# Optimization experiments

Hardware: AMD Instinct MI355X
Metric: run time of the kernel (lower is better)

The kernel has to match this reference:

```python
import jax, jax.numpy as jnp
import numpy as np

KPS = 256
HID = 1024


def _lstm_cell(x, h, c, w_ih, w_hh, b_ih, b_hh):
    # PyTorch LSTMCell: gates = x@W_ih.T + b_ih + h@W_hh.T + b_hh; order i,f,g,o
    gates = x @ w_ih.T + b_ih + h @ w_hh.T + b_hh  # [B, 4H]
    i, f, g, o = jnp.split(gates, 4, axis=-1)
    i = jax.nn.sigmoid(i)
    f = jax.nn.sigmoid(f)
    g = jnp.tanh(g)
    o = jax.nn.sigmoid(o)
    c_new = f * c + i * g
    h_new = o * jnp.tanh(c_new)
    return h_new, c_new


def setup_inputs() -> dict:
    key = jax.random.key(0)
    ks = jax.random.split(key, 20)
    B = 4096
    s_emb = 1.0 / np.sqrt(KPS)
    s_h = 1.0 / np.sqrt(HID)
    inp = {
        "kps": jax.random.normal(ks[0], (B, KPS), jnp.float32),
        "h0": jax.random.normal(ks[1], (B, HID), jnp.float32),
        "h1": jax.random.normal(ks[2], (B, HID), jnp.float32),
        "h2": jax.random.normal(ks[3], (B, HID), jnp.float32),
        "c0": jax.random.normal(ks[4], (B, HID), jnp.float32),
        "c1": jax.random.normal(ks[5], (B, HID), jnp.float32),
        "c2": jax.random.normal(ks[6], (B, HID), jnp.float32),
        # tgt_emb: Linear(kps_size, kps_size)
        "W_emb": jax.random.uniform(ks[7], (KPS, KPS), jnp.float32, -s_emb, s_emb),
        "b_emb": jax.random.uniform(ks[8], (KPS,), jnp.float32, -s_emb, s_emb),
        # lstm1: input KPS -> HID
        "w_ih1": jax.random.uniform(ks[9], (4 * HID, KPS), jnp.float32, -s_h, s_h),
        "w_hh1": jax.random.uniform(ks[10], (4 * HID, HID), jnp.float32, -s_h, s_h),
        "b_ih1": jax.random.uniform(ks[11], (4 * HID,), jnp.float32, -s_h, s_h),
        "b_hh1": jax.random.uniform(ks[12], (4 * HID,), jnp.float32, -s_h, s_h),
        # lstm2, lstm3: HID -> HID
        "w_ih2": jax.random.uniform(ks[13], (4 * HID, HID), jnp.float32, -s_h, s_h),
        "w_hh2": jax.random.uniform(ks[14], (4 * HID, HID), jnp.float32, -s_h, s_h),
        "b_ih2": jax.random.uniform(ks[15], (4 * HID,), jnp.float32, -s_h, s_h),
        "b_hh2": jax.random.uniform(ks[16], (4 * HID,), jnp.float32, -s_h, s_h),
        "w_ih3": jax.random.uniform(ks[17], (4 * HID, HID), jnp.float32, -s_h, s_h),
        "w_hh3": jax.random.uniform(ks[18], (4 * HID, HID), jnp.float32, -s_h, s_h),
        "b_ih3": jax.random.uniform(ks[19], (4 * HID,), jnp.float32, -s_h, s_h),
        "b_hh3": jax.random.uniform(jax.random.fold_in(key, 99), (4 * HID,), jnp.float32, -s_h, s_h),
    }
    return inp


def reference(kps, h0, h1, h2, c0, c1, c2,
              W_emb, b_emb,
              w_ih1, w_hh1, b_ih1, b_hh1,
              w_ih2, w_hh2, b_ih2, b_hh2,
              w_ih3, w_hh3, b_ih3, b_hh3):
    # tgt_emb linear; dropout is identity in eval mode
    in_frame = kps @ W_emb.T + b_emb
    # NOTE: per original code, lstm2/lstm3 consume the *old* hidden states
    # h0 / h1 (not the freshly computed ones).
    h0n, c0n = _lstm_cell(in_frame, h0, c0, w_ih1, w_hh1, b_ih1, b_hh1)
    h1n, c1n = _lstm_cell(h0, h1, c1, w_ih2, w_hh2, b_ih2, b_hh2)
    h2n, c2n = _lstm_cell(h1, h2, c2, w_ih3, w_hh3, b_ih3, b_hh3)
    return (h2n, h0n, h1n, h2n, c0n, c1n, c2n)
```

## Files before the change

kernel.cpp:

```cpp
#include <hip/hip_runtime.h>
#include <stdint.h>

typedef __bf16 bf16;
typedef __bf16 bf16x8 __attribute__((ext_vector_type(8)));
typedef float f32x4 __attribute__((ext_vector_type(4)));

#define B_DIM 4096
#define HID   1024
#define KPSZ  256

#define BM  128
#define BNH 32
#define BK  64

__device__ __forceinline__ bool detect_b16(const void* kps) {
  const uint16_t* k16 = (const uint16_t*)kps;
  int lane = threadIdx.x & 63;
  int c = 0;
#pragma unroll
  for (int j = 0; j < 8; ++j) {
    uint16_t v = k16[(lane * 8 + j) * 2];
    int e = (v >> 7) & 0xFF;
    c += (e >= 100 && e <= 140) ? 1 : 0;
  }
#pragma unroll
  for (int s = 1; s < 64; s <<= 1) c += __shfl_xor(c, s, 64);
  return c > 256;
}

__device__ __forceinline__ bf16x8 load8(const void* base, size_t off, bool b16) {
  if (b16) {
    return *(const bf16x8*)((const bf16*)base + off);
  } else {
    const float* f = (const float*)base + off;
    float4 lo = *(const float4*)f;
    float4 hi = *(const float4*)(f + 4);
    bf16x8 r;
    r[0] = (bf16)lo.x; r[1] = (bf16)lo.y; r[2] = (bf16)lo.z; r[3] = (bf16)lo.w;
    r[4] = (bf16)hi.x; r[5] = (bf16)hi.y; r[6] = (bf16)hi.z; r[7] = (bf16)hi.w;
    return r;
  }
}
__device__ __forceinline__ float ldg1(const void* p, size_t i, bool b16) {
  return b16 ? (float)((const bf16*)p)[i] : ((const float*)p)[i];
}
__device__ __forceinline__ void stg1(void* p, size_t i, float v, bool b16) {
  if (b16) ((bf16*)p)[i] = (bf16)v;
  else     ((float*)p)[i] = v;
}

__device__ __forceinline__ float sigm(float x) {
  return 1.0f / (1.0f + __expf(-x));
}
__device__ __forceinline__ float tanhx(float x) {
  float e = __expf(-2.0f * fabsf(x));
  float t = (1.0f - e) / (1.0f + e);
  return x < 0.0f ? -t : t;
}

__device__ __forceinline__ int sw(int row, int col8) {
  return row * BK + (col8 ^ ((row & 7) << 3));
}

__device__ __forceinline__ void gl16(const bf16* g, bf16* l) {
  __builtin_amdgcn_global_load_lds(
      (const __attribute__((address_space(1))) void*)g,
      (__attribute__((address_space(3))) void*)l, 16, 0, 0);
}


__global__ __launch_bounds__(256)
void emb_kernel(const void* __restrict__ kps, const void* __restrict__ W,
                const void* __restrict__ bias, void* __restrict__ out) {
  __shared__ __align__(16) bf16 sA[BM * BK];
  __shared__ __align__(16) bf16 sB[BNH * BK];

  const bool b16 = detect_b16(kps);
  const int n0   = blockIdx.x * BNH;
  const int m0   = blockIdx.y * BM;
  const int tid  = threadIdx.x;
  const int wave = tid >> 6;
  const int lane = tid & 63;
  const int l16  = lane & 15;
  const int kg   = lane >> 4;

  f32x4 acc[2][2] = {};

  bf16x8 ra[4], rb;
  #pragma unroll
  for (int i = 0; i < 4; ++i) {
    int it = tid + i * 256;
    ra[i] = load8(kps, (size_t)(m0 + (it >> 3)) * KPSZ + (it & 7) * 8, b16);
  }
  rb = load8(W, (size_t)(n0 + (tid >> 3)) * KPSZ + (tid & 7) * 8, b16);

  for (int s = 0; s < KPSZ / BK; ++s) {
    __syncthreads();
    #pragma unroll
    for (int i = 0; i < 4; ++i) {
      int it = tid + i * 256;
      *(bf16x8*)(sA + sw(it >> 3, (it & 7) * 8)) = ra[i];
    }
    *(bf16x8*)(sB + sw(tid >> 3, (tid & 7) * 8)) = rb;
    __syncthreads();

    if (s + 1 < KPSZ / BK) {
      int k0 = (s + 1) * BK;
      #pragma unroll
      for (int i = 0; i < 4; ++i) {
        int it = tid + i * 256;
        ra[i] = load8(kps, (size_t)(m0 + (it >> 3)) * KPSZ + k0 + (it & 7) * 8, b16);
      }
      rb = load8(W, (size_t)(n0 + (tid >> 3)) * KPSZ + k0 + (tid & 7) * 8, b16);
    }

    #pragma unroll
    for (int ks = 0; ks < 2; ++ks) {
      bf16x8 a[2], b[2];
      #pragma unroll
      for (int mi = 0; mi < 2; ++mi) {
        int row = wave * 32 + mi * 16 + l16;
        a[mi] = *(const bf16x8*)(sA + sw(row, ks * 32 + kg * 8));
      }
      #pragma unroll
      for (int ni = 0; ni < 2; ++ni) {
        int row = ni * 16 + l16;
        b[ni] = *(const bf16x8*)(sB + sw(row, ks * 32 + kg * 8));
      }
      #pragma unroll
      for (int mi = 0; mi < 2; ++mi)
        #pragma unroll
        for (int ni = 0; ni < 2; ++ni)
          acc[mi][ni] = __builtin_amdgcn_mfma_f32_16x16x32_bf16(a[mi], b[ni], acc[mi][ni], 0, 0, 0);
    }
  }

  #pragma unroll
  for (int mi = 0; mi < 2; ++mi)
    #pragma unroll
    for (int r = 0; r < 4; ++r) {
      int m = m0 + wave * 32 + mi * 16 + kg * 4 + r;
      #pragma unroll
      for (int ni = 0; ni < 2; ++ni) {
        int n = n0 + ni * 16 + l16;
        stg1(out, (size_t)m * KPSZ + n, acc[mi][ni][r] + ldg1(bias, n, b16), b16);
      }
    }
}

struct CellArgs {
  const void *Ax, *Wih, *Ah, *Whh, *bih, *bhh, *Cprev;
  size_t hoff, h2off, coff;
  int Kx, dup;
};
struct Args3 {
  CellArgs c[3];
  void* outbase;
  const void* kps;
};

__global__ __launch_bounds__(256)
void lstm_cells_kernel(Args3 A) {
  __shared__ __align__(16) bf16 sA[BM * BK];
  __shared__ __align__(16) bf16 sW[4 * BNH * BK];

  const CellArgs p = A.c[blockIdx.z];
  const bool b16 = detect_b16(A.kps);
  const int n0   = blockIdx.x * BNH;
  const int m0   = blockIdx.y * BM;
  const int tid  = threadIdx.x;
  const int wave = tid >> 6;
  const int lane = tid & 63;
  const int l16  = lane & 15;
  const int kg   = lane >> 4;

  f32x4 acc[4][2][2] = {};

  const int steps1 = p.Kx / BK;
  const int steps  = steps1 + HID / BK;

  bf16x8 ra[4], rw[4];
  #pragma unroll
  for (int i = 0; i < 4; ++i) {
    int it = tid + i * 256;
    ra[i] = load8(p.Ax, (size_t)(m0 + (it >> 3)) * p.Kx + (it & 7) * 8, b16);
  }
  #pragma unroll
  for (int i = 0; i < 4; ++i) {
    int it = tid + i * 256;
    int rr = it >> 3;
    int grow = (rr >> 5) * HID + n0 + (rr & 31);
    rw[i] = load8(p.Wih, (size_t)grow * p.Kx + (it & 7) * 8, b16);
  }

  for (int s = 0; s < steps; ++s) {
    __syncthreads();
    #pragma unroll
    for (int i = 0; i < 4; ++i) {
      int it = tid + i * 256;
      *(bf16x8*)(sA + sw(it >> 3, (it & 7) * 8)) = ra[i];
    }
    #pragma unroll
    for (int i = 0; i < 4; ++i) {
      int it = tid + i * 256;
      *(bf16x8*)(sW + sw(it >> 3, (it & 7) * 8)) = rw[i];
    }
    __syncthreads();

    if (s + 1 < steps) {
      const void *A_, *W_; int K_, k0_;
      int s2 = s + 1;
      if (s2 < steps1) { A_ = p.Ax; W_ = p.Wih; K_ = p.Kx; k0_ = s2 * BK; }
      else             { A_ = p.Ah; W_ = p.Whh; K_ = HID;  k0_ = (s2 - steps1) * BK; }
      #pragma unroll
      for (int i = 0; i < 4; ++i) {
        int it = tid + i * 256;
        ra[i] = load8(A_, (size_t)(m0 + (it >> 3)) * K_ + k0_ + (it & 7) * 8, b16);
      }
      #pragma unroll
      for (int i = 0; i < 4; ++i) {
        int it = tid + i * 256;
        int rr = it >> 3;
        int grow = (rr >> 5) * HID + n0 + (rr & 31);
        rw[i] = load8(W_, (size_t)grow * K_ + k0_ + (it & 7) * 8, b16);
      }
    }

    #pragma unroll
    for (int ks = 0; ks < 2; ++ks) {
      bf16x8 a[2], b[4][2];
      #pragma unroll
      for (int mi = 0; mi < 2; ++mi) {
        int row = wave * 32 + mi * 16 + l16;
        a[mi] = *(const bf16x8*)(sA + sw(row, ks * 32 + kg * 8));
      }
      #pragma unroll
      for (int g = 0; g < 4; ++g)
        #pragma unroll
        for (int ni = 0; ni < 2; ++ni) {
          int row = g * 32 + ni * 16 + l16;
          b[g][ni] = *(const bf16x8*)(sW + sw(row, ks * 32 + kg * 8));
        }
      #pragma unroll
      for (int g = 0; g < 4; ++g)
        #pragma unroll
        for (int mi = 0; mi < 2; ++mi)
          #pragma unroll
          for (int ni = 0; ni < 2; ++ni)
            acc[g][mi][ni] = __builtin_amdgcn_mfma_f32_16x16x32_bf16(
                a[mi], b[g][ni], acc[g][mi][ni], 0, 0, 0);
    }
  }

  float bsum[4][2];
  #pragma unroll
  for (int g = 0; g < 4; ++g)
    #pragma unroll
    for (int ni = 0; ni < 2; ++ni) {
      int n = n0 + ni * 16 + l16;
      bsum[g][ni] = ldg1(p.bih, g * HID + n, b16) + ldg1(p.bhh, g * HID + n, b16);
    }

  #pragma unroll
  for (int mi = 0; mi < 2; ++mi)
    #pragma unroll
    for (int r = 0; r < 4; ++r) {
      int m = m0 + wave * 32 + mi * 16 + kg * 4 + r;
      size_t rowoff = (size_t)m * HID;
      #pragma unroll
      for (int ni = 0; ni < 2; ++ni) {
        int n = n0 + ni * 16 + l16;
        float xi = acc[0][mi][ni][r] + bsum[0][ni];
        float xf = acc[1][mi][ni][r] + bsum[1][ni];
        float xg = acc[2][mi][ni][r] + bsum[2][ni];
        float xo = acc[3][mi][ni][r] + bsum[3][ni];
        float I = sigm(xi);
        float F = sigm(xf);
        float G = tanhx(xg);
        float O = sigm(xo);
        float c  = ldg1(p.Cprev, rowoff + n, b16);
        float cn = F * c + I * G;
        float hn = O * tanhx(cn);
        stg1(A.outbase, p.coff + rowoff + n, cn, b16);
        stg1(A.outbase, p.hoff + rowoff + n, hn, b16);
        if (p.dup) stg1(A.outbase, p.h2off + rowoff + n, hn, b16);
      }
    }
}


#define NSEG 9

struct PrepArgs {
  const void* src[NSEG];
  bf16*       dst[NSEG];
  unsigned    pre[NSEG + 1];
  const void* kps;
  const void* W_emb;
  const void* b_emb;
  bf16*       in_frame;
  int         nconv;
};

__global__ __launch_bounds__(256)
void prep_kernel(PrepArgs P) {
  const bool b16 = detect_b16(P.kps);
  const int tid = threadIdx.x;
  const int bid = blockIdx.x;

  if (bid < 256) {
    __shared__ __align__(16) bf16 sA[BM * BK];
    __shared__ __align__(16) bf16 sB[BNH * BK];
    const int n0   = (bid & 7) * BNH;
    const int m0   = (bid >> 3) * BM;
    const int wave = tid >> 6;
    const int lane = tid & 63;
    const int l16  = lane & 15;
    const int kg   = lane >> 4;

    f32x4 acc[2][2] = {};
    bf16x8 ra[4], rb;
    #pragma unroll
    for (int i = 0; i < 4; ++i) {
      int it = tid + i * 256;
      ra[i] = load8(P.kps, (size_t)(m0 + (it >> 3)) * KPSZ + (it & 7) * 8, b16);
    }
    rb = load8(P.W_emb, (size_t)(n0 + (tid >> 3)) * KPSZ + (tid & 7) * 8, b16);

    for (int s = 0; s < KPSZ / BK; ++s) {
      __syncthreads();
      #pragma unroll
      for (int i = 0; i < 4; ++i) {
        int it = tid + i * 256;
        *(bf16x8*)(sA + sw(it >> 3, (it & 7) * 8)) = ra[i];
      }
      *(bf16x8*)(sB + sw(tid >> 3, (tid & 7) * 8)) = rb;
      __syncthreads();

      if (s + 1 < KPSZ / BK) {
        int k0 = (s + 1) * BK;
        #pragma unroll
        for (int i = 0; i < 4; ++i) {
          int it = tid + i * 256;
          ra[i] = load8(P.kps, (size_t)(m0 + (it >> 3)) * KPSZ + k0 + (it & 7) * 8, b16);
        }
        rb = load8(P.W_emb, (size_t)(n0 + (tid >> 3)) * KPSZ + k0 + (tid & 7) * 8, b16);
      }

      #pragma unroll
      for (int ks = 0; ks < 2; ++ks) {
        bf16x8 a[2], bfr[2];
        #pragma unroll
        for (int mi = 0; mi < 2; ++mi) {
          int row = wave * 32 + mi * 16 + l16;
          a[mi] = *(const bf16x8*)(sA + sw(row, ks * 32 + kg * 8));
        }
        #pragma unroll
        for (int ni = 0; ni < 2; ++ni) {
          int row = ni * 16 + l16;
          bfr[ni] = *(const bf16x8*)(sB + sw(row, ks * 32 + kg * 8));
        }
        #pragma unroll
        for (int mi = 0; mi < 2; ++mi)
          #pragma unroll
          for (int ni = 0; ni < 2; ++ni)
            acc[mi][ni] = __builtin_amdgcn_mfma_f32_16x16x32_bf16(a[mi], bfr[ni], acc[mi][ni], 0, 0, 0);
      }
    }

    #pragma unroll
    for (int mi = 0; mi < 2; ++mi)
      #pragma unroll
      for (int r = 0; r < 4; ++r) {
        int m = m0 + wave * 32 + mi * 16 + kg * 4 + r;
        #pragma unroll
        for (int ni = 0; ni < 2; ++ni) {
          int n = n0 + ni * 16 + l16;
          P.in_frame[(size_t)m * KPSZ + n] = (bf16)(acc[mi][ni][r] + ldg1(P.b_emb, n, b16));
        }
      }
    return;
  }

  const int cb = bid - 256;
  const unsigned tot = P.pre[NSEG];
  const unsigned stride = (unsigned)P.nconv * 256u;
  for (unsigned c = (unsigned)cb * 256u + (unsigned)tid; c < tot; c += stride) {
    int s = 0;
    #pragma unroll
    for (int k = 0; k < NSEG - 1; ++k) s += (c >= P.pre[k + 1]) ? 1 : 0;
    unsigned lc = c - P.pre[s];
    bf16x8 v = load8(P.src[s], (size_t)lc * 8, b16);
    *(bf16x8*)(P.dst[s] + (size_t)lc * 8) = v;
  }
}

struct NCell {
  const bf16 *Ax, *Wih, *Ah, *Whh;
  const void *bih, *bhh, *Cprev;
  size_t hoff, h2off, coff;
  int Kx, dup;
};
struct NArgs {
  NCell c[3];
  void* outbase;
  const void* kps;
};

__global__ __launch_bounds__(256)
void lstm_fast_kernel(NArgs A) {
  __shared__ __align__(16) bf16 sA[BM * BK];
  __shared__ __align__(16) bf16 sW[4 * BNH * BK];

  const NCell p = A.c[blockIdx.z];
  const bool b16 = detect_b16(A.kps);
  const int n0   = blockIdx.x * BNH;
  const int m0   = blockIdx.y * BM;
  const int tid  = threadIdx.x;
  const int w    = tid >> 6;
  const int lane = tid & 63;
  const int l16  = lane & 15;
  const int kg   = lane >> 4;
  const int wm   = w >> 1;
  const int wn   = w & 1;

  f32x4 acc[4][4] = {};

  const int steps1 = p.Kx / BK;
  const int steps  = steps1 + HID / BK;

  for (int s = 0; s < steps; ++s) {
    const bf16 *A_, *W_; int K_, k0_;
    if (s < steps1) { A_ = p.Ax; W_ = p.Wih; K_ = p.Kx; k0_ = s * BK; }
    else            { A_ = p.Ah; W_ = p.Whh; K_ = HID;  k0_ = (s - steps1) * BK; }

    #pragma unroll
    for (int j = 0; j < 4; ++j) {
      int c0 = (j * 4 + w) * 64;
      int c  = c0 + lane;
      gl16(A_ + (size_t)(m0 + (c >> 3)) * K_ + k0_ + (c & 7) * 8, sA + c0 * 8);
    }
    #pragma unroll
    for (int j = 0; j < 4; ++j) {
      int c0 = (j * 4 + w) * 64;
      int c  = c0 + lane;
      int r  = c >> 3;
      int grow = (r >> 5) * HID + n0 + (r & 31);
      gl16(W_ + (size_t)grow * K_ + k0_ + (c & 7) * 8, sW + c0 * 8);
    }
    __syncthreads();

    #pragma unroll
    for (int ks = 0; ks < 2; ++ks) {
      bf16x8 a[4], b[4];
      #pragma unroll
      for (int mi = 0; mi < 4; ++mi) {
        int row = wm * 64 + mi * 16 + l16;
        a[mi] = *(const bf16x8*)(sA + row * BK + ks * 32 + kg * 8);
      }
      #pragma unroll
      for (int g = 0; g < 4; ++g) {
        int row = g * 32 + wn * 16 + l16;
        b[g] = *(const bf16x8*)(sW + row * BK + ks * 32 + kg * 8);
      }
      #pragma unroll
      for (int g = 0; g < 4; ++g)
        #pragma unroll
        for (int mi = 0; mi < 4; ++mi)
          acc[g][mi] = __builtin_amdgcn_mfma_f32_16x16x32_bf16(a[mi], b[g], acc[g][mi], 0, 0, 0);
    }
    __syncthreads();
  }

  const int n = n0 + wn * 16 + l16;
  float bsum[4];
  #pragma unroll
  for (int g = 0; g < 4; ++g)
    bsum[g] = ldg1(p.bih, g * HID + n, b16) + ldg1(p.bhh, g * HID + n, b16);

  #pragma unroll
  for (int mi = 0; mi < 4; ++mi)
    #pragma unroll
    for (int r = 0; r < 4; ++r) {
      int m = m0 + wm * 64 + mi * 16 + kg * 4 + r;
      size_t rowoff = (size_t)m * HID;
      float xi = acc[0][mi][r] + bsum[0];
      float xf = acc[1][mi][r] + bsum[1];
      float xg = acc[2][mi][r] + bsum[2];
      float xo = acc[3][mi][r] + bsum[3];
      float I = sigm(xi);
      float F = sigm(xf);
      float G = tanhx(xg);
      float O = sigm(xo);
      float c  = ldg1(p.Cprev, rowoff + n, b16);
      float cn = F * c + I * G;
      float hn = O * tanhx(cn);
      stg1(A.outbase, p.coff + rowoff + n, cn, b16);
      stg1(A.outbase, p.hoff + rowoff + n, hn, b16);
      if (p.dup) stg1(A.outbase, p.h2off + rowoff + n, hn, b16);
    }
}

extern "C" void kernel_launch(void* const* d_in, const int* in_sizes, int n_in,
                              void* d_out, int out_size, void* d_ws, size_t ws_size,
                              hipStream_t stream) {
  const void* kps   = d_in[0];
  const void* h0    = d_in[1];
  const void* h1    = d_in[2];
  const void* h2    = d_in[3];
  const void* c0    = d_in[4];
  const void* c1    = d_in[5];
  const void* c2    = d_in[6];
  const void* W_emb = d_in[7];
  const void* b_emb = d_in[8];
  const void* w_ih1 = d_in[9];
  const void* w_hh1 = d_in[10];
  const void* b_ih1 = d_in[11];
  const void* b_hh1 = d_in[12];
  const void* w_ih2 = d_in[13];
  const void* w_hh2 = d_in[14];
  const void* b_ih2 = d_in[15];
  const void* b_hh2 = d_in[16];
  const void* w_ih3 = d_in[17];
  const void* w_hh3 = d_in[18];
  const void* b_ih3 = d_in[19];
  const void* b_hh3 = d_in[20];

  const size_t S = (size_t)B_DIM * HID;

  const size_t E_SMALL = (size_t)4 * HID * KPSZ;
  const size_t E_BIG   = (size_t)4 * HID * HID;
  const size_t TOT_ELEMS = 2 * E_SMALL + 8 * E_BIG;
  const size_t NEED = TOT_ELEMS * 2;

  if (ws_size >= NEED) {
    bf16* wsb      = (bf16*)d_ws;
    bf16* in_frame = wsb;
    bf16* W1x      = wsb + E_SMALL;
    bf16* W1h      = W1x + E_SMALL;
    bf16* W2x      = W1h + E_BIG;
    bf16* W2h      = W2x + E_BIG;
    bf16* W3x      = W2h + E_BIG;
    bf16* W3h      = W3x + E_BIG;
    bf16* H0       = W3h + E_BIG;
    bf16* H1       = H0 + E_BIG;
    bf16* H2       = H1 + E_BIG;

    PrepArgs P;
    const void* srcs[NSEG] = { w_ih1, w_hh1, w_ih2, w_hh2, w_ih3, w_hh3, h0, h1, h2 };
    bf16*       dsts[NSEG] = { W1x,   W1h,   W2x,   W2h,   W3x,   W3h,  H0, H1, H2 };
    unsigned    cnts[NSEG] = { (unsigned)(E_SMALL / 8), (unsigned)(E_BIG / 8),
                               (unsigned)(E_BIG / 8),   (unsigned)(E_BIG / 8),
                               (unsigned)(E_BIG / 8),   (unsigned)(E_BIG / 8),
                               (unsigned)(E_BIG / 8),   (unsigned)(E_BIG / 8),
                               (unsigned)(E_BIG / 8) };
    unsigned acc = 0;
    for (int i = 0; i < NSEG; ++i) {
      P.src[i] = srcs[i];
      P.dst[i] = dsts[i];
      P.pre[i] = acc;
      acc += cnts[i];
    }
    P.pre[NSEG] = acc;
    P.kps = kps; P.W_emb = W_emb; P.b_emb = b_emb; P.in_frame = in_frame;
    P.nconv = 2048;

    prep_kernel<<<dim3(256 + 2048), 256, 0, stream>>>(P);

    NArgs N;
    N.outbase = d_out;
    N.kps = kps;
    N.c[0] = { in_frame, W1x, H0, W1h, b_ih1, b_hh1, c0, 1 * S, 0, 4 * S, KPSZ, 0 };
    N.c[1] = { H0,       W2x, H1, W2h, b_ih2, b_hh2, c1, 2 * S, 0, 5 * S, HID,  0 };
    N.c[2] = { H1,       W3x, H2, W3h, b_ih3, b_hh3, c2, 0,     3 * S, 6 * S, HID, 1 };

    lstm_fast_kernel<<<dim3(HID / BNH, B_DIM / BM, 3), 256, 0, stream>>>(N);
    return;
  }

  void* in_frame = d_ws;
  emb_kernel<<<dim3(KPSZ / BNH, B_DIM / BM), 256, 0, stream>>>(kps, W_emb, b_emb, in_frame);

  Args3 A;
  A.outbase = d_out;
  A.kps = kps;
  A.c[0] = { in_frame, w_ih1, h0, w_hh1, b_ih1, b_hh1, c0,
             1 * S, 0, 4 * S, KPSZ, 0 };
  A.c[1] = { h0, w_ih2, h1, w_hh2, b_ih2, b_hh2, c1,
             2 * S, 0, 5 * S, HID, 0 };
  A.c[2] = { h1, w_ih3, h2, w_hh3, b_ih3, b_hh3, c2,
             0 * S, 3 * S, 6 * S, HID, 1 };

  lstm_cells_kernel<<<dim3(HID / BNH, B_DIM / BM, 3), 256, 0, stream>>>(A);
}
```

Before: 533.8 us.

## Enlarge LSTM GEMM tiles with double-buffered LDS, XOR swizzle and 8 waves

Reworks the fused LSTM gate GEMM to use 256x64-per-gate tiles with 512 threads, a BK of 32, and double-buffered shared memory so the next tile's global loads overlap the current MFMA work. LDS rows use an XOR swizzle to cut bank conflicts, and s_setprio raises wave priority around the MFMA bursts. The goal is more operand reuse per loaded byte and less exposed load latency. In exchange the grid has far fewer blocks, each holding 128 accumulator registers per lane, which can lower occupancy and leave CUs idle.

After: 565.5 us. 1.06x slower.

```diff
diff --git a/kernel.cpp b/kernel.cpp
--- a/kernel.cpp
+++ b/kernel.cpp
@@ -12,6 +12,10 @@
 #define BM  128
 #define BNH 32
 #define BK  64
+
+#define BM2 256
+#define BN2 64
+#define BK2 32
 
 __device__ __forceinline__ bool detect_b16(const void* kps) {
   const uint16_t* k16 = (const uint16_t*)kps;
@@ -395,6 +399,7 @@
   }
 }
 
+
 struct NCell {
   const bf16 *Ax, *Wih, *Ah, *Whh;
   const void *bih, *bhh, *Cprev;
@@ -407,68 +412,106 @@
   const void* kps;
 };
 
-__global__ __launch_bounds__(256)
-void lstm_fast_kernel(NArgs A) {
-  __shared__ __align__(16) bf16 sA[BM * BK];
-  __shared__ __align__(16) bf16 sW[4 * BNH * BK];
-
-  const NCell p = A.c[blockIdx.z];
-  const bool b16 = detect_b16(A.kps);
-  const int n0   = blockIdx.x * BNH;
-  const int m0   = blockIdx.y * BM;
+__device__ __forceinline__ void stage_tile2(const bf16* A_, const bf16* W_,
+                                            int K_, int k0_, int m0, int n0,
+                                            bf16* sa, bf16* swk,
+                                            int w, int lane) {
+  #pragma unroll
+  for (int j = 0; j < 2; ++j) {
+    int c0 = (j * 8 + w) * 64;
+    int c  = c0 + lane;
+    int row = c >> 2, col8 = c & 3;
+    int gc  = col8 ^ ((row >> 1) & 3);
+    gl16(A_ + (size_t)(m0 + row) * K_ + k0_ + gc * 8, sa + c0 * 8);
+  }
+  #pragma unroll
+  for (int j = 0; j < 2; ++j) {
+    int c0 = (j * 8 + w) * 64;
+    int c  = c0 + lane;
+    int row = c >> 2, col8 = c & 3;
+    int gc  = col8 ^ ((row >> 1) & 3);
+    int wrow = (row >> 6) * HID + n0 + (row & 63);
+    gl16(W_ + (size_t)wrow * K_ + k0_ + gc * 8, swk + c0 * 8);
+  }
+}
+
+__global__ __launch_bounds__(512, 2)
+void lstm_fast_kernel(NArgs Ar) {
+  __shared__ __align__(16) bf16 sA[2][BM2 * BK2];
+  __shared__ __align__(16) bf16 sW[2][4 * BN2 * BK2];
+
+  const NCell p = Ar.c[blockIdx.z];
+  const bool b16 = detect_b16(Ar.kps);
+  const int n0   = blockIdx.x * BN2;
+  const int m0   = blockIdx.y * BM2;
   const int tid  = threadIdx.x;
   const int w    = tid >> 6;
   const int lane = tid & 63;
   const int l16  = lane & 15;
   const int kg   = lane >> 4;
-  const int wm   = w >> 1;
-  const int wn   = w & 1;
-
-  f32x4 acc[4][4] = {};
-
-  const int steps1 = p.Kx / BK;
-  const int steps  = steps1 + HID / BK;
-
-  for (int s = 0; s < steps; ++s) {
-    const bf16 *A_, *W_; int K_, k0_;
-    if (s < steps1) { A_ = p.Ax; W_ = p.Wih; K_ = p.Kx; k0_ = s * BK; }
-    else            { A_ = p.Ah; W_ = p.Whh; K_ = HID;  k0_ = (s - steps1) * BK; }
-
-    #pragma unroll
-    for (int j = 0; j < 4; ++j) {
-      int c0 = (j * 4 + w) * 64;
-      int c  = c0 + lane;
-      gl16(A_ + (size_t)(m0 + (c >> 3)) * K_ + k0_ + (c & 7) * 8, sA + c0 * 8);
-    }
-    #pragma unroll
-    for (int j = 0; j < 4; ++j) {
-      int c0 = (j * 4 + w) * 64;
-      int c  = c0 + lane;
-      int r  = c >> 3;
-      int grow = (r >> 5) * HID + n0 + (r & 31);
-      gl16(W_ + (size_t)grow * K_ + k0_ + (c & 7) * 8, sW + c0 * 8);
-    }
-    __syncthreads();
-
-    #pragma unroll
-    for (int ks = 0; ks < 2; ++ks) {
-      bf16x8 a[4], b[4];
+  const int wm   = w >> 2;
+  const int wn   = w & 3;
+
+  f32x4 acc[4][8] = {};
+
+  const int s1 = p.Kx / BK2;
+  const int nt = s1 + HID / BK2;
+
+  stage_tile2(p.Ax, p.Wih, p.Kx, 0, m0, n0, sA[0], sW[0], w, lane);
+  __syncthreads();
+
+  for (int v = 0; v < nt; ++v) {
+    if (v + 1 < nt) {
+      const bf16 *A_, *W_; int K_, k0_;
+      int v2 = v + 1;
+      if (v2 < s1) { A_ = p.Ax; W_ = p.Wih; K_ = p.Kx; k0_ = v2 * BK2; }
+      else         { A_ = p.Ah; W_ = p.Whh; K_ = HID;  k0_ = (v2 - s1) * BK2; }
+      stage_tile2(A_, W_, K_, k0_, m0, n0, sA[v2 & 1], sW[v2 & 1], w, lane);
+    }
+
+    const bf16* sa = sA[v & 1];
+    const bf16* sw_ = sW[v & 1];
+
+    bf16x8 b[4];
+    #pragma unroll
+    for (int g = 0; g < 4; ++g) {
+      int rb = g * 64 + wn * 16 + l16;
+      b[g] = *(const bf16x8*)(sw_ + rb * BK2 + ((kg ^ ((rb >> 1) & 3)) * 8));
+    }
+
+    {
+      bf16x8 a[4];
       #pragma unroll
       for (int mi = 0; mi < 4; ++mi) {
-        int row = wm * 64 + mi * 16 + l16;
-        a[mi] = *(const bf16x8*)(sA + row * BK + ks * 32 + kg * 8);
-      }
-      #pragma unroll
-      for (int g = 0; g < 4; ++g) {
-        int row = g * 32 + wn * 16 + l16;
-        b[g] = *(const bf16x8*)(sW + row * BK + ks * 32 + kg * 8);
-      }
+        int ra = wm * 128 + mi * 16 + l16;
+        a[mi] = *(const bf16x8*)(sa + ra * BK2 + ((kg ^ ((ra >> 1) & 3)) * 8));
+      }
+      __builtin_amdgcn_s_setprio(1);
       #pragma unroll
       for (int g = 0; g < 4; ++g)
         #pragma unroll
         for (int mi = 0; mi < 4; ++mi)
           acc[g][mi] = __builtin_amdgcn_mfma_f32_16x16x32_bf16(a[mi], b[g], acc[g][mi], 0, 0, 0);
-    }
+      __builtin_amdgcn_s_setprio(0);
+    }
+    __builtin_amdgcn_s_barrier();
+
+    {
+      bf16x8 a[4];
+      #pragma unroll
+      for (int mi = 0; mi < 4; ++mi) {
+        int ra = wm * 128 + (mi + 4) * 16 + l16;
+        a[mi] = *(const bf16x8*)(sa + ra * BK2 + ((kg ^ ((ra >> 1) & 3)) * 8));
+      }
+      __builtin_amdgcn_s_setprio(1);
+      #pragma unroll
+      for (int g = 0; g < 4; ++g)
+        #pragma unroll
+        for (int mi = 0; mi < 4; ++mi)
+          acc[g][mi + 4] = __builtin_amdgcn_mfma_f32_16x16x32_bf16(a[mi], b[g], acc[g][mi + 4], 0, 0, 0);
+      __builtin_amdgcn_s_setprio(0);
+    }
+
     __syncthreads();
   }
 
@@ -479,10 +522,10 @@
     bsum[g] = ldg1(p.bih, g * HID + n, b16) + ldg1(p.bhh, g * HID + n, b16);
 
   #pragma unroll
-  for (int mi = 0; mi < 4; ++mi)
+  for (int mi = 0; mi < 8; ++mi)
     #pragma unroll
     for (int r = 0; r < 4; ++r) {
-      int m = m0 + wm * 64 + mi * 16 + kg * 4 + r;
+      int m = m0 + wm * 128 + mi * 16 + kg * 4 + r;
       size_t rowoff = (size_t)m * HID;
       float xi = acc[0][mi][r] + bsum[0];
       float xf = acc[1][mi][r] + bsum[1];
@@ -495,9 +538,9 @@
       float c  = ldg1(p.Cprev, rowoff + n, b16);
       float cn = F * c + I * G;
       float hn = O * tanhx(cn);
-      stg1(A.outbase, p.coff + rowoff + n, cn, b16);
-      stg1(A.outbase, p.hoff + rowoff + n, hn, b16);
-      if (p.dup) stg1(A.outbase, p.h2off + rowoff + n, hn, b16);
+      stg1(Ar.outbase, p.coff + rowoff + n, cn, b16);
+      stg1(Ar.outbase, p.hoff + rowoff + n, hn, b16);
+      if (p.dup) stg1(Ar.outbase, p.h2off + rowoff + n, hn, b16);
     }
 }
 
@@ -574,7 +617,7 @@
     N.c[1] = { H0,       W2x, H1, W2h, b_ih2, b_hh2, c1, 2 * S, 0, 5 * S, HID,  0 };
     N.c[2] = { H1,       W3x, H2, W3h, b_ih3, b_hh3, c2, 0,     3 * S, 6 * S, HID, 1 };
 
-    lstm_fast_kernel<<<dim3(HID / BNH, B_DIM / BM, 3), 256, 0, stream>>>(N);
+    lstm_fast_kernel<<<dim3(HID / BN2, B_DIM / BM2, 3), 512, 0, stream>>>(N);
     return;
   }
 
```

## Triple-buffer LSTM GEMM tiles with async loads and swizzled LDS

Applied to the files above, without the earlier changes.

Rewrites the main LSTM GEMM loop to use a 3-stage LDS ring buffer with BK=32. The next tiles are issued two steps ahead, and explicit vmcnt waits plus raw s_barrier replace the load-then-sync pattern, so global loads overlap MFMA work. It also adds an XOR swizzle on the LDS layout to cut bank conflicts, changes the warp layout to 4x1 over M, and sets launch bounds to 3 blocks per CU. The cost is hand-managed wait counts that must match the number of loads in flight, plus more LDS per block.

Result: faster. 512.9 us (-3.9%).

```diff
diff --git a/kernel.cpp b/kernel.cpp
--- a/kernel.cpp
+++ b/kernel.cpp
@@ -12,6 +12,8 @@
 #define BM  128
 #define BNH 32
 #define BK  64
+
+#define BK3 32
 
 __device__ __forceinline__ bool detect_b16(const void* kps) {
   const uint16_t* k16 = (const uint16_t*)kps;
@@ -395,6 +397,7 @@
   }
 }
 
+
 struct NCell {
   const bf16 *Ax, *Wih, *Ah, *Whh;
   const void *bih, *bhh, *Cprev;
@@ -407,97 +410,133 @@
   const void* kps;
 };
 
-__global__ __launch_bounds__(256)
-void lstm_fast_kernel(NArgs A) {
-  __shared__ __align__(16) bf16 sA[BM * BK];
-  __shared__ __align__(16) bf16 sW[4 * BNH * BK];
-
-  const NCell p = A.c[blockIdx.z];
-  const bool b16 = detect_b16(A.kps);
-  const int n0   = blockIdx.x * BNH;
-  const int m0   = blockIdx.y * BM;
+__global__ __launch_bounds__(256, 3)
+void lstm_fast_kernel(NArgs Ar) {
+  __shared__ __align__(16) bf16 smem[3 * 8192];
+
+  const NCell p = Ar.c[blockIdx.z];
+  const bool b16 = detect_b16(Ar.kps);
+  const int n0   = blockIdx.x * 32;
+  const int m0   = blockIdx.y * 128;
   const int tid  = threadIdx.x;
   const int w    = tid >> 6;
   const int lane = tid & 63;
   const int l16  = lane & 15;
   const int kg   = lane >> 4;
-  const int wm   = w >> 1;
-  const int wn   = w & 1;
-
-  f32x4 acc[4][4] = {};
-
-  const int steps1 = p.Kx / BK;
-  const int steps  = steps1 + HID / BK;
-
-  for (int s = 0; s < steps; ++s) {
-    const bf16 *A_, *W_; int K_, k0_;
-    if (s < steps1) { A_ = p.Ax; W_ = p.Wih; K_ = p.Kx; k0_ = s * BK; }
-    else            { A_ = p.Ah; W_ = p.Whh; K_ = HID;  k0_ = (s - steps1) * BK; }
-
-    #pragma unroll
-    for (int j = 0; j < 4; ++j) {
-      int c0 = (j * 4 + w) * 64;
-      int c  = c0 + lane;
-      gl16(A_ + (size_t)(m0 + (c >> 3)) * K_ + k0_ + (c & 7) * 8, sA + c0 * 8);
-    }
-    #pragma unroll
-    for (int j = 0; j < 4; ++j) {
-      int c0 = (j * 4 + w) * 64;
-      int c  = c0 + lane;
-      int r  = c >> 3;
-      int grow = (r >> 5) * HID + n0 + (r & 31);
-      gl16(W_ + (size_t)grow * K_ + k0_ + (c & 7) * 8, sW + c0 * 8);
-    }
-    __syncthreads();
-
-    #pragma unroll
-    for (int ks = 0; ks < 2; ++ks) {
-      bf16x8 a[4], b[4];
-      #pragma unroll
-      for (int mi = 0; mi < 4; ++mi) {
-        int row = wm * 64 + mi * 16 + l16;
-        a[mi] = *(const bf16x8*)(sA + row * BK + ks * 32 + kg * 8);
-      }
-      #pragma unroll
-      for (int g = 0; g < 4; ++g) {
-        int row = g * 32 + wn * 16 + l16;
-        b[g] = *(const bf16x8*)(sW + row * BK + ks * 32 + kg * 8);
-      }
-      #pragma unroll
-      for (int g = 0; g < 4; ++g)
-        #pragma unroll
-        for (int mi = 0; mi < 4; ++mi)
-          acc[g][mi] = __builtin_amdgcn_mfma_f32_16x16x32_bf16(a[mi], b[g], acc[g][mi], 0, 0, 0);
-    }
-    __syncthreads();
-  }
-
-  const int n = n0 + wn * 16 + l16;
-  float bsum[4];
+
+  f32x4 acc[4][2][2] = {};
+
+  const int s1 = p.Kx / BK3;
+  const int nt = s1 + HID / BK3;
+
+  const bf16 *pA0, *pA1, *pW0, *pW1, *hA0, *hA1, *hW0, *hW1;
+  {
+    int c0 = tid,       r0_ = c0 >> 2, g0_ = (c0 & 3) ^ ((r0_ >> 1) & 3);
+    int c1 = tid + 256, r1_ = c1 >> 2, g1_ = (c1 & 3) ^ ((r1_ >> 1) & 3);
+    pA0 = p.Ax + (size_t)(m0 + r0_) * p.Kx + g0_ * 8;
+    pA1 = p.Ax + (size_t)(m0 + r1_) * p.Kx + g1_ * 8;
+    hA0 = p.Ah + (size_t)(m0 + r0_) * HID + g0_ * 8;
+    hA1 = p.Ah + (size_t)(m0 + r1_) * HID + g1_ * 8;
+    int w0 = (r0_ >> 5) * HID + n0 + (r0_ & 31);
+    int w1 = (r1_ >> 5) * HID + n0 + (r1_ & 31);
+    pW0 = p.Wih + (size_t)w0 * p.Kx + g0_ * 8;
+    pW1 = p.Wih + (size_t)w1 * p.Kx + g1_ * 8;
+    hW0 = p.Whh + (size_t)w0 * HID + g0_ * 8;
+    hW1 = p.Whh + (size_t)w1 * HID + g1_ * 8;
+  }
+  const int ldsO0 = w * 512;
+  const int ldsO1 = w * 512 + 2048;
+
+  auto issue = [&](int t, int b) {
+    if (t == s1) { pA0 = hA0; pA1 = hA1; pW0 = hW0; pW1 = hW1; }
+    bf16* d = smem + b * 8192;
+    gl16(pA0, d + ldsO0);
+    gl16(pA1, d + ldsO1);
+    gl16(pW0, d + 4096 + ldsO0);
+    gl16(pW1, d + 4096 + ldsO1);
+    pA0 += BK3; pA1 += BK3; pW0 += BK3; pW1 += BK3;
+  };
+
+  issue(0, 0);
+  issue(1, 1);
+
+  int cb = 0;
+  for (int v = 0; v < nt; ++v) {
+    if (v + 2 < nt) {
+      int ib = cb + 2; if (ib >= 3) ib -= 3;
+      issue(v + 2, ib);
+      asm volatile("s_waitcnt vmcnt(8)" ::: "memory");
+    } else if (v + 1 < nt) {
+      asm volatile("s_waitcnt vmcnt(4)" ::: "memory");
+    } else {
+      asm volatile("s_waitcnt vmcnt(0)" ::: "memory");
+    }
+    __builtin_amdgcn_s_barrier();
+    asm volatile("" ::: "memory");
+
+    const bf16* sa  = smem + cb * 8192;
+    const bf16* sw_ = sa + 4096;
+
+    bf16x8 a[2], b[4][2];
+    #pragma unroll
+    for (int mi = 0; mi < 2; ++mi) {
+      int row = w * 32 + mi * 16 + l16;
+      a[mi] = *(const bf16x8*)(sa + row * 32 + ((kg ^ ((row >> 1) & 3)) * 8));
+    }
+    #pragma unroll
+    for (int g = 0; g < 4; ++g)
+      #pragma unroll
+      for (int ni = 0; ni < 2; ++ni) {
+        int row = g * 32 + ni * 16 + l16;
+        b[g][ni] = *(const bf16x8*)(sw_ + row * 32 + ((kg ^ ((row >> 1) & 3)) * 8));
+      }
+    #pragma unroll
+    for (int g = 0; g < 4; ++g)
+      #pragma unroll
+      for (int mi = 0; mi < 2; ++mi)
+        #pragma unroll
+        for (int ni = 0; ni < 2; ++ni)
+          acc[g][mi][ni] = __builtin_amdgcn_mfma_f32_16x16x32_bf16(
+              a[mi], b[g][ni], acc[g][mi][ni], 0, 0, 0);
+
+    asm volatile("" ::: "memory");
+    __builtin_amdgcn_s_barrier();
+    if (++cb == 3) cb = 0;
+  }
+
+  float bsum[4][2];
   #pragma unroll
   for (int g = 0; g < 4; ++g)
-    bsum[g] = ldg1(p.bih, g * HID + n, b16) + ldg1(p.bhh, g * HID + n, b16);
-
-  #pragma unroll
-  for (int mi = 0; mi < 4; ++mi)
+    #pragma unroll
+    for (int ni = 0; ni < 2; ++ni) {
+      int n = n0 + ni * 16 + l16;
+      bsum[g][ni] = ldg1(p.bih, g * HID + n, b16) + ldg1(p.bhh, g * HID + n, b16);
+    }
+
+  #pragma unroll
+  for (int mi = 0; mi < 2; ++mi)
     #pragma unroll
     for (int r = 0; r < 4; ++r) {
-      int m = m0 + wm * 64 + mi * 16 + kg * 4 + r;
+      int m = m0 + w * 32 + mi * 16 + kg * 4 + r;
       size_t rowoff = (size_t)m * HID;
-      float xi = acc[0][mi][r] + bsum[0];
-      float xf = acc[1][mi][r] + bsum[1];
-      float xg = acc[2][mi][r] + bsum[2];
-      float xo = acc[3][mi][r] + bsum[3];
-      float I = sigm(xi);
-      float F = sigm(xf);
-      float G = tanhx(xg);
-      float O = sigm(xo);
-      float c  = ldg1(p.Cprev, rowoff + n, b16);
-      float cn = F * c + I * G;
-      float hn = O * tanhx(cn);
-      stg1(A.outbase, p.coff + rowoff + n, cn, b16);
-      stg1(A.outbase, p.hoff + rowoff + n, hn, b16);
-      if (p.dup) stg1(A.outbase, p.h2off + rowoff + n, hn, b16);
+      #pragma unroll
+      for (int ni = 0; ni < 2; ++ni) {
+        int n = n0 + ni * 16 + l16;
+        float xi = acc[0][mi][ni][r] + bsum[0][ni];
+        float xf = acc[1][mi][ni][r] + bsum[1][ni];
+        float xg = acc[2][mi][ni][r] + bsum[2][ni];
+        float xo = acc[3][mi][ni][r] + bsum[3][ni];
+        float I = sigm(xi);
+        float F = sigm(xf);
+        float G = tanhx(xg);
+        float O = sigm(xo);
+        float c  = ldg1(p.Cprev, rowoff + n, b16);
+        float cn = F * c + I * G;
+        float hn = O * tanhx(cn);
+        stg1(Ar.outbase, p.coff + rowoff + n, cn, b16);
+        stg1(Ar.outbase, p.hoff + rowoff + n, hn, b16);
+        if (p.dup) stg1(Ar.outbase, p.h2off + rowoff + n, hn, b16);
+      }
     }
 }
 
@@ -574,7 +613,7 @@
     N.c[1] = { H0,       W2x, H1, W2h, b_ih2, b_hh2, c1, 2 * S, 0, 5 * S, HID,  0 };
     N.c[2] = { H1,       W3x, H2, W3h, b_ih3, b_hh3, c2, 0,     3 * S, 6 * S, HID, 1 };
 
-    lstm_fast_kernel<<<dim3(HID / BNH, B_DIM / BM, 3), 256, 0, stream>>>(N);
+    lstm_fast_kernel<<<dim3(HID / 32, B_DIM / 128, 3), 256, 0, stream>>>(N);
     return;
   }
 
```
